# Kernel optimization log

Hardware: AMD Instinct MI355X
Metric: run time of the kernel (lower is better)

The kernel has to match this reference:

```python
import jax, jax.numpy as jnp
import numpy as np

NUM_BINS = 256          # CLAHE histogram bins (kornia default)
GRID = (8, 8)           # CLAHE tile grid (kornia default)
LOG_GAIN = 2.5          # module init arg
CLIP_LIMIT = 1.0        # module init arg


def normalize_in_range(x, lo=0.0, hi=1.0):
    mn = x.min()
    mx = x.max()
    return (x - mn) / (mx - mn) * (hi - lo) + lo


def adjust_log(x, gain):
    # skimage/kornia log adjust: gain * log2(1 + x)
    return gain * jnp.log2(1.0 + x)


def equalize_clahe(x, clip_limit=CLIP_LIMIT, grid=GRID):
    B, C, H, W = x.shape
    gh, gw = grid
    th = -(-H // gh)   # ceil tile height
    tw = -(-W // gw)   # ceil tile width
    Hp, Wp = th * gh, tw * gw
    if (Hp, Wp) != (H, W):
        x = jnp.pad(x, ((0, 0), (0, 0), (0, Hp - H), (0, Wp - W)), mode='reflect')

    # bin index per pixel (values saturated into [0,1])
    xc = jnp.clip(x, 0.0, 1.0)
    bins = jnp.clip((xc * NUM_BINS).astype(jnp.int32), 0, NUM_BINS - 1)  # B,C,Hp,Wp

    # --- per-tile histograms: (B*C*gh*gw) tiles of th*tw pixels ---
    tb = bins.reshape(B, C, gh, th, gw, tw).transpose(0, 1, 2, 4, 3, 5)
    tb = tb.reshape(B * C * gh * gw, th * tw)
    hist = jax.vmap(lambda ix: jnp.bincount(ix, length=NUM_BINS))(tb).astype(jnp.float32)

    pixels = th * tw
    # --- clip + uniform redistribution of excess ---
    if clip_limit > 0:
        clip_max = max(int(clip_limit * pixels // NUM_BINS), 1)
        excess = jnp.maximum(hist - clip_max, 0.0).sum(-1)
        hist = jnp.minimum(hist, float(clip_max))
        redist = jnp.floor(excess / NUM_BINS)
        residual = excess - redist * NUM_BINS
        hist = hist + redist[:, None] \
             + (jnp.arange(NUM_BINS)[None, :] < residual[:, None]).astype(hist.dtype)

    # --- CDF -> LUT in [0, 255] ---
    lut = jnp.clip(jnp.floor(jnp.cumsum(hist, -1) * ((NUM_BINS - 1) / pixels)), 0.0, NUM_BINS - 1.0)
    lut = lut.reshape(B, C, gh, gw, NUM_BINS)

    # --- bilinear interpolation between the 4 neighboring tile LUTs ---
    iy = jnp.arange(Hp, dtype=jnp.float32)
    ty = (iy + 0.5) / th - 0.5
    y0f = jnp.floor(ty)
    wy = (ty - y0f)[:, None]                                   # Hp x 1
    y0 = jnp.clip(y0f.astype(jnp.int32), 0, gh - 1)[:, None]
    y1 = jnp.clip(y0f.astype(jnp.int32) + 1, 0, gh - 1)[:, None]

    ix = jnp.arange(Wp, dtype=jnp.float32)
    tx = (ix + 0.5) / tw - 0.5
    x0f = jnp.floor(tx)
    wx = (tx - x0f)[None, :]
    x0 = jnp.clip(x0f.astype(jnp.int32), 0, gw - 1)[None, :]
    x1 = jnp.clip(x0f.astype(jnp.int32) + 1, 0, gw - 1)[None, :]

    flat_lut = lut.reshape(-1)
    bidx = jnp.arange(B)[:, None, None, None]
    cidx = jnp.arange(C)[None, :, None, None]

    def gather(yi, xi):
        idx = (((bidx * C + cidx) * gh + yi) * gw + xi) * NUM_BINS + bins
        return flat_lut[idx]

    v = (1.0 - wy) * ((1.0 - wx) * gather(y0, x0) + wx * gather(y0, x1)) \
        + wy * ((1.0 - wx) * gather(y1, x0) + wx * gather(y1, x1))
    out = v / (NUM_BINS - 1)
    return out[..., :H, :W]


def setup_inputs() -> dict:
    key = jax.random.key(0)
    x = jax.random.uniform(key, (8, 1, 2048, 2048), dtype=jnp.float32)
    return {"x": x}


def reference(x):
    shape = x.shape
    x = normalize_in_range(x, 0.0, 1.0)
    x = adjust_log(x, gain=LOG_GAIN)
    x = equalize_clahe(x, clip_limit=CLIP_LIMIT)
    x = normalize_in_range(x, 0.0, 1.0)
    return x.reshape(shape)
```

## Files before the change

kernel.cpp:

```cpp
#include <hip/hip_runtime.h>

#define NIMG 8
#define IMH 2048
#define IMW 2048
#define GH 8
#define GW 8
#define NBINS 256
#define NTPI 64
#define CLIP_MAXF 256.0f
#define LUT_SCALE 0.0038909912109375f
#define LOG_GAIN_F 2.5f

#define MM_BLOCKS 2048

typedef float f32x4 __attribute__((ext_vector_type(4)));

__device__ __forceinline__ int pix_bin(float v, float mn, float inv_den) {
    float xn = (v - mn) * inv_den;
    float t  = LOG_GAIN_F * __log2f(1.0f + xn);
    float xc = fminf(fmaxf(t, 0.0f), 1.0f);
    int b = (int)(xc * 256.0f);
    return min(max(b, 0), 255);
}

__device__ __forceinline__ void mm4(float4 v, float& mn, float& mx) {
    mn = fminf(mn, fminf(fminf(v.x, v.y), fminf(v.z, v.w)));
    mx = fmaxf(mx, fmaxf(fmaxf(v.x, v.y), fmaxf(v.z, v.w)));
}

template <int NWAVES>
__device__ __forceinline__ void block_minmax_all(float& mn, float& mx, int t) {
#pragma unroll
    for (int m = 32; m >= 1; m >>= 1) {
        mn = fminf(mn, __shfl_xor(mn, m, 64));
        mx = fmaxf(mx, __shfl_xor(mx, m, 64));
    }
    __shared__ float smn[NWAVES], smx[NWAVES];
    int wid = t >> 6, lid = t & 63;
    if (lid == 0) { smn[wid] = mn; smx[wid] = mx; }
    __syncthreads();
    mn = smn[0]; mx = smx[0];
#pragma unroll
    for (int i = 1; i < NWAVES; i++) { mn = fminf(mn, smn[i]); mx = fmaxf(mx, smx[i]); }
}

__global__ __launch_bounds__(256) void k_minmax_in(const float4* __restrict__ x,
                                                   float2* __restrict__ red) {
    int t = threadIdx.x;
    size_t base = (size_t)blockIdx.x * 4096 + t;
    float mn0 = 3.4e38f, mx0 = -3.4e38f;
    float mn1 = 3.4e38f, mx1 = -3.4e38f;
    float mn2 = 3.4e38f, mx2 = -3.4e38f;
    float mn3 = 3.4e38f, mx3 = -3.4e38f;
#pragma unroll
    for (int k = 0; k < 16; k += 4) {
        float4 v0 = x[base + (size_t)(k + 0) * 256];
        float4 v1 = x[base + (size_t)(k + 1) * 256];
        float4 v2 = x[base + (size_t)(k + 2) * 256];
        float4 v3 = x[base + (size_t)(k + 3) * 256];
        mm4(v0, mn0, mx0); mm4(v1, mn1, mx1); mm4(v2, mn2, mx2); mm4(v3, mn3, mx3);
    }
    float mn = fminf(fminf(mn0, mn1), fminf(mn2, mn3));
    float mx = fmaxf(fmaxf(mx0, mx1), fmaxf(mx2, mx3));
    block_minmax_all<4>(mn, mx, t);
    if (t == 0) red[blockIdx.x] = make_float2(mn, mx);
}

__global__ __launch_bounds__(1024) void k_hist(const float* __restrict__ x,
                                               const float2* __restrict__ red1,
                                               float* __restrict__ lut,
                                               uchar4* __restrict__ bins) {
    int t = threadIdx.x;

    float mn, mx;
    {
        float2 p0 = red1[t];
        float2 p1 = red1[t + 1024];
        mn = fminf(p0.x, p1.x);
        mx = fmaxf(p0.y, p1.y);
        block_minmax_all<16>(mn, mx, t);
    }
    float inv_den = 1.0f / (mx - mn);

    __shared__ unsigned sh[NBINS];
    if (t < NBINS) sh[t] = 0u;
    __syncthreads();

    int tile = blockIdx.x;
    int img  = blockIdx.y;
    int ty = tile >> 3, tx = tile & 7;

    size_t base = ((size_t)img * IMH + (size_t)ty * 256) * IMW + (size_t)tx * 256;
    const float* xt = x + base;
    int lid = t & 63;
    int rowoff = t >> 6;
    int c4 = t & 63;

    unsigned hotacc = 0;
    for (int it = 0; it < 16; ++it) {
        int r = (it << 4) + rowoff;
        float4 v = *(const float4*)(xt + (size_t)r * IMW + (c4 << 2));
        int b[4];
        b[0] = pix_bin(v.x, mn, inv_den);
        b[1] = pix_bin(v.y, mn, inv_den);
        b[2] = pix_bin(v.z, mn, inv_den);
        b[3] = pix_bin(v.w, mn, inv_den);
#pragma unroll
        for (int j = 0; j < 4; j++) {
            bool hot = (b[j] == 255);
            unsigned long long m = __ballot(hot);
            if (!hot) atomicAdd(&sh[b[j]], 1u);
            hotacc += (unsigned)__popcll(m);
        }
        uchar4 q;
        q.x = (unsigned char)b[0]; q.y = (unsigned char)b[1];
        q.z = (unsigned char)b[2]; q.w = (unsigned char)b[3];
        bins[(base + (size_t)r * IMW + (size_t)(c4 << 2)) >> 2] = q;
    }
    if (lid == 0 && hotacc) atomicAdd(&sh[255], hotacc);
    __syncthreads();

    int wid = t >> 6;
    float h = 0.0f, ex = 0.0f;
    if (t < NBINS) {
        h = (float)sh[t];
        ex = fmaxf(h - CLIP_MAXF, 0.0f);
    }
    float s = ex;
#pragma unroll
    for (int m = 1; m < 64; m <<= 1) s += __shfl_xor(s, m, 64);
    __shared__ float wpart[16];
    if (lid == 0) wpart[wid] = s;
    __syncthreads();
    float excess = wpart[0] + wpart[1] + wpart[2] + wpart[3];

    h = fminf(h, CLIP_MAXF);
    float redist   = floorf(excess * (1.0f / 256.0f));
    float residual = excess - redist * 256.0f;
    h = h + redist + (((float)t < residual) ? 1.0f : 0.0f);

    float c = h;
#pragma unroll
    for (int m = 1; m < 64; m <<= 1) {
        float o = __shfl_up(c, m, 64);
        if (lid >= m) c += o;
    }
    __shared__ float wsum[16];
    if (lid == 63) wsum[wid] = c;
    __syncthreads();
    if (t < NBINS) {
        float off = 0.0f;
        for (int i = 0; i < wid; i++) off += wsum[i];
        c += off;
        float l = fminf(floorf(c * LUT_SCALE), 255.0f);
        l = fmaxf(l, 0.0f);
        lut[((size_t)img * NTPI + tile) * NBINS + t] = l;
    }
}

template <bool FINAL>
__global__ __launch_bounds__(256) void k_apply(const uchar4* __restrict__ bins,
                                               const float* __restrict__ lut,
                                               float2* __restrict__ red2,
                                               float4* __restrict__ out) {
    __shared__ float4 Lq[NBINS];
    int t = threadIdx.x;

    float pmn = 0.f, oscale = 1.f;
    if (FINAL) {
        float vmn = 3.4e38f, vmx = -3.4e38f;
#pragma unroll
        for (int k = 0; k < 8; k++) {
            float2 p = red2[t + k * 256];
            vmn = fminf(vmn, p.x);
            vmx = fmaxf(vmx, p.y);
        }
        block_minmax_all<4>(vmn, vmx, t);
        pmn = vmn * (1.0f / 255.0f);
        float pmx = vmx * (1.0f / 255.0f);
        oscale = 1.0f / (pmx - pmn);
    }

    int qx = blockIdx.x, qy = blockIdx.y, img = blockIdx.z;
    const float* lb = lut + (size_t)img * NTPI * NBINS;
    {
        int ty2 = qy >> 1, tx2 = qx >> 1;
        int yA = (qy & 1) ? ty2 : max(ty2 - 1, 0);
        int yB = (qy & 1) ? min(ty2 + 1, GH - 1) : ty2;
        int xA = (qx & 1) ? tx2 : max(tx2 - 1, 0);
        int xB = (qx & 1) ? min(tx2 + 1, GW - 1) : tx2;
        float4 g;
        g.x = lb[(size_t)(yA * GW + xA) * NBINS + t];
        g.y = lb[(size_t)(yA * GW + xB) * NBINS + t];
        g.z = lb[(size_t)(yB * GW + xA) * NBINS + t];
        g.w = lb[(size_t)(yB * GW + xB) * NBINS + t];
        Lq[t] = g;
    }
    __syncthreads();

    float vmnl = 3.4e38f, vmxl = -3.4e38f;
    int gy0 = qy << 7, gx0 = qx << 7;
    int rowoff = t >> 5;
    int c4 = t & 31;
    int ix0 = gx0 + (c4 << 2);

    float wxv[4];
#pragma unroll
    for (int j = 0; j < 4; j++) {
        float txf = ((float)(ix0 + j) + 0.5f) * (1.0f / 256.0f) - 0.5f;
        wxv[j] = txf - floorf(txf);
    }

    for (int it = 0; it < 16; ++it) {
        int r = (it << 3) + rowoff;
        int iy = gy0 + r;
        size_t pidx = ((size_t)img * IMH + iy) * IMW + ix0;
        uchar4 q = bins[pidx >> 2];
        int b[4] = {q.x, q.y, q.z, q.w};

        float tyf = ((float)iy + 0.5f) * (1.0f / 256.0f) - 0.5f;
        float wy = tyf - floorf(tyf);
        float4 o;
        float* op = &o.x;
#pragma unroll
        for (int j = 0; j < 4; j++) {
            float4 g = Lq[b[j]];
            float a = g.x + wxv[j] * (g.y - g.x);
            float bb = g.z + wxv[j] * (g.w - g.z);
            float v = a + wy * (bb - a);
            if (FINAL) {
                float p = v * (1.0f / 255.0f);
                op[j] = (p - pmn) * oscale;
            } else {
                vmnl = fminf(vmnl, v);
                vmxl = fmaxf(vmxl, v);
            }
        }
        if (FINAL) {
            f32x4 ov = {o.x, o.y, o.z, o.w};
            __builtin_nontemporal_store(ov, (f32x4*)&out[pidx >> 2]);
        }
    }

    if (!FINAL) {
        block_minmax_all<4>(vmnl, vmxl, t);
        if (t == 0) {
            int bid = (img * 16 + qy) * 16 + qx;
            red2[bid] = make_float2(vmnl, vmxl);
        }
    }
}

extern "C" void kernel_launch(void* const* d_in, const int* in_sizes, int n_in,
                              void* d_out, int out_size, void* d_ws, size_t ws_size,
                              hipStream_t stream) {
    const float* x = (const float*)d_in[0];
    float4* out = (float4*)d_out;

    unsigned char* ws = (unsigned char*)d_ws;
    float* lut    = (float*)(ws + 64);
    float2* red1  = (float2*)(ws + 64 + 512 * 1024);
    float2* red2  = (float2*)(ws + 64 + 512 * 1024 + 16384);
    uchar4* bins  = (uchar4*)(ws + 1024 * 1024);

    k_minmax_in<<<dim3(MM_BLOCKS), dim3(256), 0, stream>>>((const float4*)x, red1);
    k_hist<<<dim3(NTPI, NIMG), dim3(1024), 0, stream>>>(x, red1, lut, bins);
    dim3 qgrid(16, 16, NIMG);
    k_apply<false><<<qgrid, dim3(256), 0, stream>>>(bins, lut, red2, out);
    k_apply<true><<<qgrid, dim3(256), 0, stream>>>(bins, lut, red2, out);
}
```

Measured before the change: 109.3 us.

## Batch loads, replace per-pixel ballots with shuffle reduction, fold output normalization into LUT

```diff
diff --git a/kernel.cpp b/kernel.cpp
--- a/kernel.cpp
+++ b/kernel.cpp
@@ -48,20 +48,16 @@
                                                    float2* __restrict__ red) {
     int t = threadIdx.x;
     size_t base = (size_t)blockIdx.x * 4096 + t;
-    float mn0 = 3.4e38f, mx0 = -3.4e38f;
-    float mn1 = 3.4e38f, mx1 = -3.4e38f;
-    float mn2 = 3.4e38f, mx2 = -3.4e38f;
-    float mn3 = 3.4e38f, mx3 = -3.4e38f;
-#pragma unroll
-    for (int k = 0; k < 16; k += 4) {
-        float4 v0 = x[base + (size_t)(k + 0) * 256];
-        float4 v1 = x[base + (size_t)(k + 1) * 256];
-        float4 v2 = x[base + (size_t)(k + 2) * 256];
-        float4 v3 = x[base + (size_t)(k + 3) * 256];
-        mm4(v0, mn0, mx0); mm4(v1, mn1, mx1); mm4(v2, mn2, mx2); mm4(v3, mn3, mx3);
-    }
-    float mn = fminf(fminf(mn0, mn1), fminf(mn2, mn3));
-    float mx = fmaxf(fmaxf(mx0, mx1), fmaxf(mx2, mx3));
+    float mn = 3.4e38f, mx = -3.4e38f;
+#pragma unroll
+    for (int half = 0; half < 2; ++half) {
+        float4 v[8];
+#pragma unroll
+        for (int k = 0; k < 8; ++k)
+            v[k] = x[base + (size_t)(half * 8 + k) * 256];
+#pragma unroll
+        for (int k = 0; k < 8; ++k) mm4(v[k], mn, mx);
+    }
     block_minmax_all<4>(mn, mx, t);
     if (t == 0) red[blockIdx.x] = make_float2(mn, mx);
 }
@@ -96,28 +92,37 @@
     int rowoff = t >> 6;
     int c4 = t & 63;
 
-    unsigned hotacc = 0;
-    for (int it = 0; it < 16; ++it) {
-        int r = (it << 4) + rowoff;
-        float4 v = *(const float4*)(xt + (size_t)r * IMW + (c4 << 2));
-        int b[4];
-        b[0] = pix_bin(v.x, mn, inv_den);
-        b[1] = pix_bin(v.y, mn, inv_den);
-        b[2] = pix_bin(v.z, mn, inv_den);
-        b[3] = pix_bin(v.w, mn, inv_den);
+    int hotcnt = 0;
+    for (int it = 0; it < 16; it += 2) {
+        int r0 = (it << 4) + rowoff;
+        int r1 = ((it + 1) << 4) + rowoff;
+        float4 va = *(const float4*)(xt + (size_t)r0 * IMW + (c4 << 2));
+        float4 vb = *(const float4*)(xt + (size_t)r1 * IMW + (c4 << 2));
+
+        int ba[4], bb[4];
+        ba[0] = pix_bin(va.x, mn, inv_den); ba[1] = pix_bin(va.y, mn, inv_den);
+        ba[2] = pix_bin(va.z, mn, inv_den); ba[3] = pix_bin(va.w, mn, inv_den);
+        bb[0] = pix_bin(vb.x, mn, inv_den); bb[1] = pix_bin(vb.y, mn, inv_den);
+        bb[2] = pix_bin(vb.z, mn, inv_den); bb[3] = pix_bin(vb.w, mn, inv_den);
+
 #pragma unroll
         for (int j = 0; j < 4; j++) {
-            bool hot = (b[j] == 255);
-            unsigned long long m = __ballot(hot);
-            if (!hot) atomicAdd(&sh[b[j]], 1u);
-            hotacc += (unsigned)__popcll(m);
-        }
-        uchar4 q;
-        q.x = (unsigned char)b[0]; q.y = (unsigned char)b[1];
-        q.z = (unsigned char)b[2]; q.w = (unsigned char)b[3];
-        bins[(base + (size_t)r * IMW + (size_t)(c4 << 2)) >> 2] = q;
-    }
-    if (lid == 0 && hotacc) atomicAdd(&sh[255], hotacc);
+            hotcnt += (ba[j] == 255);
+            if (ba[j] != 255) atomicAdd(&sh[ba[j]], 1u);
+            hotcnt += (bb[j] == 255);
+            if (bb[j] != 255) atomicAdd(&sh[bb[j]], 1u);
+        }
+        uchar4 qa, qb;
+        qa.x = (unsigned char)ba[0]; qa.y = (unsigned char)ba[1];
+        qa.z = (unsigned char)ba[2]; qa.w = (unsigned char)ba[3];
+        qb.x = (unsigned char)bb[0]; qb.y = (unsigned char)bb[1];
+        qb.z = (unsigned char)bb[2]; qb.w = (unsigned char)bb[3];
+        bins[(base + (size_t)r0 * IMW + (size_t)(c4 << 2)) >> 2] = qa;
+        bins[(base + (size_t)r1 * IMW + (size_t)(c4 << 2)) >> 2] = qb;
+    }
+#pragma unroll
+    for (int m = 1; m < 64; m <<= 1) hotcnt += __shfl_xor(hotcnt, m, 64);
+    if (lid == 0 && hotcnt) atomicAdd(&sh[255], (unsigned)hotcnt);
     __syncthreads();
 
     int wid = t >> 6;
@@ -166,7 +171,7 @@
     __shared__ float4 Lq[NBINS];
     int t = threadIdx.x;
 
-    float pmn = 0.f, oscale = 1.f;
+    float s1 = 1.0f, s2 = 0.0f;
     if (FINAL) {
         float vmn = 3.4e38f, vmx = -3.4e38f;
 #pragma unroll
@@ -176,9 +181,11 @@
             vmx = fmaxf(vmx, p.y);
         }
         block_minmax_all<4>(vmn, vmx, t);
-        pmn = vmn * (1.0f / 255.0f);
+        float pmn = vmn * (1.0f / 255.0f);
         float pmx = vmx * (1.0f / 255.0f);
-        oscale = 1.0f / (pmx - pmn);
+        float oscale = 1.0f / (pmx - pmn);
+        s1 = oscale * (1.0f / 255.0f);
+        s2 = -pmn * oscale;
     }
 
     int qx = blockIdx.x, qy = blockIdx.y, img = blockIdx.z;
@@ -190,10 +197,10 @@
         int xA = (qx & 1) ? tx2 : max(tx2 - 1, 0);
         int xB = (qx & 1) ? min(tx2 + 1, GW - 1) : tx2;
         float4 g;
-        g.x = lb[(size_t)(yA * GW + xA) * NBINS + t];
-        g.y = lb[(size_t)(yA * GW + xB) * NBINS + t];
-        g.z = lb[(size_t)(yB * GW + xA) * NBINS + t];
-        g.w = lb[(size_t)(yB * GW + xB) * NBINS + t];
+        g.x = lb[(size_t)(yA * GW + xA) * NBINS + t] * s1 + s2;
+        g.y = lb[(size_t)(yA * GW + xB) * NBINS + t] * s1 + s2;
+        g.z = lb[(size_t)(yB * GW + xA) * NBINS + t] * s1 + s2;
+        g.w = lb[(size_t)(yB * GW + xB) * NBINS + t] * s1 + s2;
         Lq[t] = g;
     }
     __syncthreads();
@@ -211,34 +218,42 @@
         wxv[j] = txf - floorf(txf);
     }
 
-    for (int it = 0; it < 16; ++it) {
-        int r = (it << 3) + rowoff;
-        int iy = gy0 + r;
-        size_t pidx = ((size_t)img * IMH + iy) * IMW + ix0;
-        uchar4 q = bins[pidx >> 2];
-        int b[4] = {q.x, q.y, q.z, q.w};
-
-        float tyf = ((float)iy + 0.5f) * (1.0f / 256.0f) - 0.5f;
-        float wy = tyf - floorf(tyf);
-        float4 o;
-        float* op = &o.x;
-#pragma unroll
-        for (int j = 0; j < 4; j++) {
-            float4 g = Lq[b[j]];
-            float a = g.x + wxv[j] * (g.y - g.x);
-            float bb = g.z + wxv[j] * (g.w - g.z);
-            float v = a + wy * (bb - a);
+    for (int it = 0; it < 16; it += 2) {
+        int r0 = (it << 3) + rowoff;
+        int r1 = ((it + 1) << 3) + rowoff;
+        int iy0 = gy0 + r0, iy1 = gy0 + r1;
+        size_t p0 = ((size_t)img * IMH + iy0) * IMW + ix0;
+        size_t p1 = ((size_t)img * IMH + iy1) * IMW + ix0;
+        uchar4 qa = bins[p0 >> 2];
+        uchar4 qb = bins[p1 >> 2];
+
+#pragma unroll
+        for (int half = 0; half < 2; ++half) {
+            uchar4 q = half ? qb : qa;
+            int iy = half ? iy1 : iy0;
+            size_t pidx = half ? p1 : p0;
+            int b[4] = {q.x, q.y, q.z, q.w};
+            float tyf = ((float)iy + 0.5f) * (1.0f / 256.0f) - 0.5f;
+            float wy = tyf - floorf(tyf);
+            float4 o;
+            float* op = &o.x;
+#pragma unroll
+            for (int j = 0; j < 4; j++) {
+                float4 g = Lq[b[j]];
+                float a = g.x + wxv[j] * (g.y - g.x);
+                float bbv = g.z + wxv[j] * (g.w - g.z);
+                float v = a + wy * (bbv - a);
+                if (FINAL) {
+                    op[j] = v;
+                } else {
+                    vmnl = fminf(vmnl, v);
+                    vmxl = fmaxf(vmxl, v);
+                }
+            }
             if (FINAL) {
-                float p = v * (1.0f / 255.0f);
-                op[j] = (p - pmn) * oscale;
-            } else {
-                vmnl = fminf(vmnl, v);
-                vmxl = fmaxf(vmxl, v);
+                f32x4 ov = {o.x, o.y, o.z, o.w};
+                __builtin_nontemporal_store(ov, (f32x4*)&out[pidx >> 2]);
             }
-        }
-        if (FINAL) {
-            f32x4 ov = {o.x, o.y, o.z, o.w};
-            __builtin_nontemporal_store(ov, (f32x4*)&out[pidx >> 2]);
         }
     }
 
```

After: 106.0 us. 3.0% less time.
